# Optimization experiments

Measured on AMD Instinct MI355X. Metric: run time of the kernel, lower is better.

## Reference

```python
import jax, jax.numpy as jnp
import numpy as np
import math

FEAT_DIM = 128
N_BANK = 1000000
K_NEG = 4096
BATCH = 256
T = 0.5
MOMENTUM = 0.5
EPS = 1e-7


def setup_inputs() -> dict:
    key = jax.random.key(0)
    k1, k2, k3, k4, k5, k6 = jax.random.split(key, 6)
    stdv = 1.0 / math.sqrt(FEAT_DIM / 3)
    memory_l = jax.random.uniform(k1, (N_BANK, FEAT_DIM), minval=-stdv, maxval=stdv, dtype=jnp.float32)
    memory_ab = jax.random.uniform(k2, (N_BANK, FEAT_DIM), minval=-stdv, maxval=stdv, dtype=jnp.float32)
    l = jax.random.normal(k3, (BATCH, FEAT_DIM), dtype=jnp.float32)
    ab = jax.random.normal(k4, (BATCH, FEAT_DIM), dtype=jnp.float32)
    y = jax.random.randint(k5, (BATCH,), 0, N_BANK, dtype=jnp.int32)
    idx = jax.random.randint(k6, (BATCH, K_NEG + 1), 0, N_BANK, dtype=jnp.int32)
    idx = idx.at[:, 0].set(y)  # positive sample in slot 0, as in torch forward
    return {"l": l, "ab": ab, "memory_l": memory_l, "memory_ab": memory_ab, "y": y, "idx": idx}


def _l2_normalize(x):
    # matches torch: x / (sqrt(sum(x^2)) + eps)
    return x / (jnp.sqrt(jnp.sum(x * x, axis=1, keepdims=True)) + EPS)


def _momentum_update(memory, y, x_norm):
    # gather rows, momentum mix, renormalize, scatter back
    pos = memory[y] * MOMENTUM + x_norm * (1.0 - MOMENTUM)          # [B, D]
    norm = jnp.sqrt(jnp.sum(pos * pos, axis=1, keepdims=True))
    return memory.at[y].set(pos / norm)


def reference(l, ab, memory_l, memory_ab, y, idx):
    outputSize = memory_l.shape[0]
    ln = _l2_normalize(l)
    abn = _l2_normalize(ab)

    # gather negatives+positive from the AB bank, score against l features
    w_ab = jax.lax.stop_gradient(memory_ab[idx])                     # [B, K+1, D]
    P_l = jnp.exp(jnp.einsum('bkd,bd->bk', w_ab, ln) / T)[..., None]  # [B, K+1, 1]
    Z_l = jnp.mean(P_l) * outputSize
    out_l = P_l / Z_l

    w_l = jax.lax.stop_gradient(memory_l[idx])                       # [B, K+1, D]
    P_ab = jnp.exp(jnp.einsum('bkd,bd->bk', w_l, abn) / T)[..., None]
    Z_ab = jnp.mean(P_ab) * outputSize
    out_ab = P_ab / Z_ab

    # momentum scatter update of the memory banks (no_grad in torch)
    new_memory_l = jax.lax.stop_gradient(_momentum_update(memory_l, y, ln))
    new_memory_ab = jax.lax.stop_gradient(_momentum_update(memory_ab, y, abn))

    return out_l, out_ab, new_memory_l, new_memory_ab
```

## Files before the change

kernel.cpp:

```cpp
#include <hip/hip_runtime.h>
#include <math.h>
#include <stdint.h>

#define FEAT   128
#define NBANK  1000000
#define KP1    4097
#define BATCH  256
#define INV_T  2.0f
#define EPS_N  1e-7f

constexpr size_t TOTP   = (size_t)BATCH * KP1;
constexpr size_t O_OUTL = 0;
constexpr size_t O_OUTA = TOTP;
constexpr size_t O_MEML = 2 * TOTP;
constexpr size_t O_MEMA = O_MEML + (size_t)NBANK * FEAT;

constexpr int RPB   = 16;
constexpr int NBUCK = NBANK / RPB;
constexpr int CAP   = 128;

constexpr size_t WS_LN   = 0;
constexpr size_t WS_ABN  = 32768;
constexpr size_t WS_INVZ = 65536;
constexpr size_t WS_PL   = 65544;
constexpr size_t WS_PA   = 65800;
constexpr size_t WS_U32  = 66560;

typedef float vfloat4 __attribute__((ext_vector_type(4)));

__device__ __forceinline__ float dot4(vfloat4 a, vfloat4 b) {
    return a.x * b.x + a.y * b.y + a.z * b.z + a.w * b.w;
}

__global__ void norm_zero_kernel(const float* __restrict__ l,
                                 const float* __restrict__ ab,
                                 float* __restrict__ ws,
                                 unsigned int* __restrict__ cnt) {
    int b    = blockIdx.x;
    int lane = threadIdx.x;
    for (int i = b * 64 + lane; i < NBUCK; i += 512 * 64) cnt[i] = 0u;
    const float* src;
    float*       dst;
    if (b < BATCH) { src = l  + (size_t)b * FEAT;            dst = ws + WS_LN  + (size_t)b * FEAT; }
    else           { src = ab + (size_t)(b - BATCH) * FEAT;  dst = ws + WS_ABN + (size_t)(b - BATCH) * FEAT; }
    float2 v = *(const float2*)(src + 2 * lane);
    float  ss = v.x * v.x + v.y * v.y;
    #pragma unroll
    for (int m = 1; m < 64; m <<= 1) ss += __shfl_xor(ss, m, 64);
    float inv = 1.0f / (sqrtf(ss) + EPS_N);
    ((float2*)dst)[lane] = make_float2(v.x * inv, v.y * inv);
}

__global__ void build_kernel(const int* __restrict__ idx,
                             unsigned int* __restrict__ cnt,
                             unsigned int* __restrict__ ent) {
    size_t stride = (size_t)gridDim.x * blockDim.x;
    for (size_t p = (size_t)blockIdx.x * blockDim.x + threadIdx.x; p < TOTP; p += stride) {
        int row = idx[p];
        int b   = (int)(p / KP1);
        int k   = (int)(p - (size_t)b * KP1);
        int bucket = row >> 4;
        unsigned int pos = atomicAdd(&cnt[bucket], 1u);
        if (pos < (unsigned int)CAP)
            ent[(size_t)bucket * CAP + pos] =
                ((unsigned int)b << 17) | ((unsigned int)k << 4) | (unsigned int)(row & 15);
    }
}

__global__ __launch_bounds__(256) void main_kernel(
        const float* __restrict__ mem_l, const float* __restrict__ mem_ab,
        const float* __restrict__ ws_f,
        const unsigned int* __restrict__ cnt,
        const unsigned int* __restrict__ ent,
        float* __restrict__ out) {
    __shared__ float ldsL[RPB * FEAT];
    __shared__ float ldsA[RPB * FEAT];
    __shared__ unsigned int sEnt[CAP];
    int blk = blockIdx.x;
    int tid = threadIdx.x;
    size_t fbase = (size_t)blk * RPB * FEAT;

    int c = min((int)cnt[blk], CAP);
    if (tid < CAP && tid < c) sEnt[tid] = ent[(size_t)blk * CAP + tid];

    const vfloat4* sl = (const vfloat4*)(mem_l  + fbase);
    const vfloat4* sa = (const vfloat4*)(mem_ab + fbase);
    vfloat4 vl[2], va[2];
    #pragma unroll
    for (int j = 0; j < 2; ++j) vl[j] = sl[j * 256 + tid];
    #pragma unroll
    for (int j = 0; j < 2; ++j) va[j] = sa[j * 256 + tid];

    vfloat4* lL = (vfloat4*)ldsL;
    vfloat4* lA = (vfloat4*)ldsA;
    #pragma unroll
    for (int j = 0; j < 2; ++j) { int i = j * 256 + tid; lL[i] = vl[j]; lA[i] = va[j]; }
    __syncthreads();

    vfloat4* dl_ = (vfloat4*)(out + O_MEML + fbase);
    vfloat4* da_ = (vfloat4*)(out + O_MEMA + fbase);
    #pragma unroll
    for (int j = 0; j < 2; ++j) { int i = j * 256 + tid; dl_[i] = vl[j]; da_[i] = va[j]; }

    int g = tid >> 4, lane16 = tid & 15;
    for (int i = g; i < c; i += 16) {
        unsigned int ev = sEnt[i];
        int rloc = (int)(ev & 15u);
        int k    = (int)((ev >> 4) & 0x1FFFu);
        int b    = (int)(ev >> 17);
        const vfloat4* ra = (const vfloat4*)(ldsA + rloc * FEAT) + lane16 * 2;
        const vfloat4* rl = (const vfloat4*)(ldsL + rloc * FEAT) + lane16 * 2;
        vfloat4 wa0 = ra[0], wa1 = ra[1];
        vfloat4 wl0 = rl[0], wl1 = rl[1];
        const vfloat4* lq = (const vfloat4*)(ws_f + WS_LN  + (size_t)b * FEAT) + lane16 * 2;
        const vfloat4* aq = (const vfloat4*)(ws_f + WS_ABN + (size_t)b * FEAT) + lane16 * 2;
        vfloat4 lv0 = lq[0], lv1 = lq[1];
        vfloat4 av0 = aq[0], av1 = aq[1];
        float dl  = dot4(wa0, lv0) + dot4(wa1, lv1);
        float dab = dot4(wl0, av0) + dot4(wl1, av1);
        #pragma unroll
        for (int m = 1; m < 16; m <<= 1) {
            dl  += __shfl_xor(dl,  m, 64);
            dab += __shfl_xor(dab, m, 64);
        }
        if (lane16 == 0) {
            out[O_OUTL + (size_t)b * KP1 + k] = __expf(dl  * INV_T);
            out[O_OUTA + (size_t)b * KP1 + k] = __expf(dab * INV_T);
        }
    }
}

__global__ void zsum_kernel(const float* __restrict__ out,
                            float* __restrict__ pl, float* __restrict__ pa) {
    __shared__ float sl[256], sa[256];
    int i = blockIdx.x, t = threadIdx.x;
    const float* bl = out + O_OUTL + (size_t)i * KP1;
    const float* ba = out + O_OUTA + (size_t)i * KP1;
    float a = 0.f, b = 0.f;
    for (int p = t; p < KP1; p += 256) { a += bl[p]; b += ba[p]; }
    sl[t] = a; sa[t] = b;
    __syncthreads();
    for (int s = 128; s > 0; s >>= 1) {
        if (t < s) { sl[t] += sl[t + s]; sa[t] += sa[t + s]; }
        __syncthreads();
    }
    if (t == 0) { pl[i] = sl[0]; pa[i] = sa[0]; }
}

__global__ void zfinal_kernel(const float* __restrict__ pl,
                              const float* __restrict__ pa,
                              float* __restrict__ invz) {
    if (threadIdx.x == 0) {
        float a = 0.f, b = 0.f;
        for (int i = 0; i < 256; ++i) { a += pl[i]; b += pa[i]; }
        float count = (float)TOTP;
        invz[0] = count / (a * (float)NBANK);
        invz[1] = count / (b * (float)NBANK);
    }
}

__global__ void scale_kernel(float* __restrict__ out, const float* __restrict__ invz) {
    float zl = invz[0], za = invz[1];
    size_t stride = (size_t)gridDim.x * blockDim.x;
    for (size_t i = (size_t)blockIdx.x * blockDim.x + threadIdx.x; i < TOTP; i += stride) {
        out[O_OUTL + i] *= zl;
        out[O_OUTA + i] *= za;
    }
}

__global__ void update_kernel(const float* __restrict__ mem_l,
                              const float* __restrict__ mem_ab,
                              const int*   __restrict__ y,
                              const float* __restrict__ ws,
                              float* __restrict__ out) {
    int b    = blockIdx.x;
    int lane = threadIdx.x;
    int row  = y[b];
    for (int j = b + 1; j < BATCH; ++j)
        if (y[j] == row) return;
    {
        float2 m = ((const float2*)(mem_l + (size_t)row * FEAT))[lane];
        float2 x = ((const float2*)(ws + WS_LN + (size_t)b * FEAT))[lane];
        float2 p = make_float2(m.x * 0.5f + x.x * 0.5f, m.y * 0.5f + x.y * 0.5f);
        float ss = p.x * p.x + p.y * p.y;
        #pragma unroll
        for (int mk = 1; mk < 64; mk <<= 1) ss += __shfl_xor(ss, mk, 64);
        float nrm = sqrtf(ss);
        ((float2*)(out + O_MEML + (size_t)row * FEAT))[lane] =
            make_float2(p.x / nrm, p.y / nrm);
    }
    {
        float2 m = ((const float2*)(mem_ab + (size_t)row * FEAT))[lane];
        float2 x = ((const float2*)(ws + WS_ABN + (size_t)b * FEAT))[lane];
        float2 p = make_float2(m.x * 0.5f + x.x * 0.5f, m.y * 0.5f + x.y * 0.5f);
        float ss = p.x * p.x + p.y * p.y;
        #pragma unroll
        for (int mk = 1; mk < 64; mk <<= 1) ss += __shfl_xor(ss, mk, 64);
        float nrm = sqrtf(ss);
        ((float2*)(out + O_MEMA + (size_t)row * FEAT))[lane] =
            make_float2(p.x / nrm, p.y / nrm);
    }
}

extern "C" void kernel_launch(void* const* d_in, const int* in_sizes, int n_in,
                              void* d_out, int out_size, void* d_ws, size_t ws_size,
                              hipStream_t stream) {
    const float* l      = (const float*)d_in[0];
    const float* ab     = (const float*)d_in[1];
    const float* mem_l  = (const float*)d_in[2];
    const float* mem_ab = (const float*)d_in[3];
    const int*   y      = (const int*)d_in[4];
    const int*   idx    = (const int*)d_in[5];
    float* out = (float*)d_out;
    float* ws  = (float*)d_ws;

    unsigned int* wsu = (unsigned int*)(ws + WS_U32);
    unsigned int* cnt = wsu;
    unsigned int* ent = wsu + NBUCK;

    norm_zero_kernel<<<dim3(2 * BATCH), dim3(64), 0, stream>>>(l, ab, ws, cnt);
    build_kernel<<<dim3(2048), dim3(256), 0, stream>>>(idx, cnt, ent);
    main_kernel<<<dim3(NBUCK), dim3(256), 0, stream>>>(
        mem_l, mem_ab, ws, cnt, ent, out);
    zsum_kernel  <<<dim3(256), dim3(256), 0, stream>>>(out, ws + WS_PL, ws + WS_PA);
    zfinal_kernel<<<dim3(1),   dim3(64),  0, stream>>>(ws + WS_PL, ws + WS_PA, ws + WS_INVZ);
    scale_kernel<<<dim3(1024), dim3(256), 0, stream>>>(out, ws + WS_INVZ);
    update_kernel<<<dim3(BATCH), dim3(64), 0, stream>>>(mem_l, mem_ab, y, ws, out);
}
```

Measured before the change: 490.7 us.

## Bucket gather entries per row and use persistent grid-stride main kernel

```diff
diff --git a/kernel.cpp b/kernel.cpp
--- a/kernel.cpp
+++ b/kernel.cpp
@@ -15,9 +15,9 @@
 constexpr size_t O_MEML = 2 * TOTP;
 constexpr size_t O_MEMA = O_MEML + (size_t)NBANK * FEAT;
 
-constexpr int RPB   = 16;
-constexpr int NBUCK = NBANK / RPB;
-constexpr int CAP   = 128;
+constexpr int CAP    = 16;
+constexpr int NTILE  = NBANK / 16;
+constexpr int GRID_M = 2048;
 
 constexpr size_t WS_LN   = 0;
 constexpr size_t WS_ABN  = 32768;
@@ -38,7 +38,7 @@
                                  unsigned int* __restrict__ cnt) {
     int b    = blockIdx.x;
     int lane = threadIdx.x;
-    for (int i = b * 64 + lane; i < NBUCK; i += 512 * 64) cnt[i] = 0u;
+    for (int i = b * 64 + lane; i < NBANK; i += 512 * 64) cnt[i] = 0u;
     const float* src;
     float*       dst;
     if (b < BATCH) { src = l  + (size_t)b * FEAT;            dst = ws + WS_LN  + (size_t)b * FEAT; }
@@ -59,11 +59,9 @@
         int row = idx[p];
         int b   = (int)(p / KP1);
         int k   = (int)(p - (size_t)b * KP1);
-        int bucket = row >> 4;
-        unsigned int pos = atomicAdd(&cnt[bucket], 1u);
+        unsigned int pos = atomicAdd(&cnt[row], 1u);
         if (pos < (unsigned int)CAP)
-            ent[(size_t)bucket * CAP + pos] =
-                ((unsigned int)b << 17) | ((unsigned int)k << 4) | (unsigned int)(row & 15);
+            ent[(size_t)row * CAP + pos] = ((unsigned int)b << 13) | (unsigned int)k;
     }
 }
 
@@ -73,59 +71,45 @@
         const unsigned int* __restrict__ cnt,
         const unsigned int* __restrict__ ent,
         float* __restrict__ out) {
-    __shared__ float ldsL[RPB * FEAT];
-    __shared__ float ldsA[RPB * FEAT];
-    __shared__ unsigned int sEnt[CAP];
-    int blk = blockIdx.x;
-    int tid = threadIdx.x;
-    size_t fbase = (size_t)blk * RPB * FEAT;
-
-    int c = min((int)cnt[blk], CAP);
-    if (tid < CAP && tid < c) sEnt[tid] = ent[(size_t)blk * CAP + tid];
-
-    const vfloat4* sl = (const vfloat4*)(mem_l  + fbase);
-    const vfloat4* sa = (const vfloat4*)(mem_ab + fbase);
-    vfloat4 vl[2], va[2];
-    #pragma unroll
-    for (int j = 0; j < 2; ++j) vl[j] = sl[j * 256 + tid];
-    #pragma unroll
-    for (int j = 0; j < 2; ++j) va[j] = sa[j * 256 + tid];
-
-    vfloat4* lL = (vfloat4*)ldsL;
-    vfloat4* lA = (vfloat4*)ldsA;
-    #pragma unroll
-    for (int j = 0; j < 2; ++j) { int i = j * 256 + tid; lL[i] = vl[j]; lA[i] = va[j]; }
-    __syncthreads();
-
-    vfloat4* dl_ = (vfloat4*)(out + O_MEML + fbase);
-    vfloat4* da_ = (vfloat4*)(out + O_MEMA + fbase);
-    #pragma unroll
-    for (int j = 0; j < 2; ++j) { int i = j * 256 + tid; dl_[i] = vl[j]; da_[i] = va[j]; }
-
-    int g = tid >> 4, lane16 = tid & 15;
-    for (int i = g; i < c; i += 16) {
-        unsigned int ev = sEnt[i];
-        int rloc = (int)(ev & 15u);
-        int k    = (int)((ev >> 4) & 0x1FFFu);
-        int b    = (int)(ev >> 17);
-        const vfloat4* ra = (const vfloat4*)(ldsA + rloc * FEAT) + lane16 * 2;
-        const vfloat4* rl = (const vfloat4*)(ldsL + rloc * FEAT) + lane16 * 2;
-        vfloat4 wa0 = ra[0], wa1 = ra[1];
-        vfloat4 wl0 = rl[0], wl1 = rl[1];
-        const vfloat4* lq = (const vfloat4*)(ws_f + WS_LN  + (size_t)b * FEAT) + lane16 * 2;
-        const vfloat4* aq = (const vfloat4*)(ws_f + WS_ABN + (size_t)b * FEAT) + lane16 * 2;
-        vfloat4 lv0 = lq[0], lv1 = lq[1];
-        vfloat4 av0 = aq[0], av1 = aq[1];
-        float dl  = dot4(wa0, lv0) + dot4(wa1, lv1);
-        float dab = dot4(wl0, av0) + dot4(wl1, av1);
-        #pragma unroll
-        for (int m = 1; m < 16; m <<= 1) {
-            dl  += __shfl_xor(dl,  m, 64);
-            dab += __shfl_xor(dab, m, 64);
-        }
-        if (lane16 == 0) {
-            out[O_OUTL + (size_t)b * KP1 + k] = __expf(dl  * INV_T);
-            out[O_OUTA + (size_t)b * KP1 + k] = __expf(dab * INV_T);
+    int tid    = threadIdx.x;
+    int g      = tid >> 4;
+    int lane16 = tid & 15;
+
+    for (int t = blockIdx.x; t < NTILE; t += GRID_M) {
+        int    row   = t * 16 + g;
+        size_t rbase = (size_t)row * FEAT;
+
+        int c = (int)cnt[row];
+
+        const vfloat4* pl = (const vfloat4*)(mem_l  + rbase) + lane16 * 2;
+        const vfloat4* pa = (const vfloat4*)(mem_ab + rbase) + lane16 * 2;
+        vfloat4 wl0 = pl[0], wl1 = pl[1];
+        vfloat4 wa0 = pa[0], wa1 = pa[1];
+
+        vfloat4* dl = (vfloat4*)(out + O_MEML + rbase) + lane16 * 2;
+        vfloat4* da = (vfloat4*)(out + O_MEMA + rbase) + lane16 * 2;
+        dl[0] = wl0; dl[1] = wl1;
+        da[0] = wa0; da[1] = wa1;
+
+        for (int e = 0; e < c && e < CAP; ++e) {
+            unsigned int ev = ent[(size_t)row * CAP + e];
+            int b = (int)(ev >> 13);
+            int k = (int)(ev & 0x1FFFu);
+            const vfloat4* lq = (const vfloat4*)(ws_f + WS_LN  + (size_t)b * FEAT) + lane16 * 2;
+            const vfloat4* aq = (const vfloat4*)(ws_f + WS_ABN + (size_t)b * FEAT) + lane16 * 2;
+            vfloat4 lv0 = lq[0], lv1 = lq[1];
+            vfloat4 av0 = aq[0], av1 = aq[1];
+            float dlv  = dot4(wa0, lv0) + dot4(wa1, lv1);
+            float dabv = dot4(wl0, av0) + dot4(wl1, av1);
+            #pragma unroll
+            for (int m = 1; m < 16; m <<= 1) {
+                dlv  += __shfl_xor(dlv,  m, 64);
+                dabv += __shfl_xor(dabv, m, 64);
+            }
+            if (lane16 == 0) {
+                out[O_OUTL + (size_t)b * KP1 + k] = __expf(dlv  * INV_T);
+                out[O_OUTA + (size_t)b * KP1 + k] = __expf(dabv * INV_T);
+            }
         }
     }
 }
@@ -216,11 +200,11 @@
 
     unsigned int* wsu = (unsigned int*)(ws + WS_U32);
     unsigned int* cnt = wsu;
-    unsigned int* ent = wsu + NBUCK;
+    unsigned int* ent = wsu + NBANK;
 
     norm_zero_kernel<<<dim3(2 * BATCH), dim3(64), 0, stream>>>(l, ab, ws, cnt);
     build_kernel<<<dim3(2048), dim3(256), 0, stream>>>(idx, cnt, ent);
-    main_kernel<<<dim3(NBUCK), dim3(256), 0, stream>>>(
+    main_kernel<<<dim3(GRID_M), dim3(256), 0, stream>>>(
         mem_l, mem_ab, ws, cnt, ent, out);
     zsum_kernel  <<<dim3(256), dim3(256), 0, stream>>>(out, ws + WS_PL, ws + WS_PA);
     zfinal_kernel<<<dim3(1),   dim3(64),  0, stream>>>(ws + WS_PL, ws + WS_PA, ws + WS_INVZ);
```

Result: slower. 679.0 us (+38.4%).

## Split bank copy+score per bank, drop LDS staging, fuse normalize with scatter update

Applied to the files above, without the earlier changes.

```diff
diff --git a/kernel.cpp b/kernel.cpp
--- a/kernel.cpp
+++ b/kernel.cpp
@@ -21,7 +21,6 @@
 
 constexpr size_t WS_LN   = 0;
 constexpr size_t WS_ABN  = 32768;
-constexpr size_t WS_INVZ = 65536;
 constexpr size_t WS_PL   = 65544;
 constexpr size_t WS_PA   = 65800;
 constexpr size_t WS_U32  = 66560;
@@ -67,66 +66,36 @@
     }
 }
 
-__global__ __launch_bounds__(256) void main_kernel(
-        const float* __restrict__ mem_l, const float* __restrict__ mem_ab,
-        const float* __restrict__ ws_f,
+__global__ __launch_bounds__(256) void copyscore_kernel(
+        const float* __restrict__ src, float* __restrict__ dst,
+        const float* __restrict__ qtab, float* __restrict__ pout,
         const unsigned int* __restrict__ cnt,
-        const unsigned int* __restrict__ ent,
-        float* __restrict__ out) {
-    __shared__ float ldsL[RPB * FEAT];
-    __shared__ float ldsA[RPB * FEAT];
-    __shared__ unsigned int sEnt[CAP];
+        const unsigned int* __restrict__ ent) {
     int blk = blockIdx.x;
     int tid = threadIdx.x;
     size_t fbase = (size_t)blk * RPB * FEAT;
 
     int c = min((int)cnt[blk], CAP);
-    if (tid < CAP && tid < c) sEnt[tid] = ent[(size_t)blk * CAP + tid];
 
-    const vfloat4* sl = (const vfloat4*)(mem_l  + fbase);
-    const vfloat4* sa = (const vfloat4*)(mem_ab + fbase);
-    vfloat4 vl[2], va[2];
-    #pragma unroll
-    for (int j = 0; j < 2; ++j) vl[j] = sl[j * 256 + tid];
-    #pragma unroll
-    for (int j = 0; j < 2; ++j) va[j] = sa[j * 256 + tid];
-
-    vfloat4* lL = (vfloat4*)ldsL;
-    vfloat4* lA = (vfloat4*)ldsA;
-    #pragma unroll
-    for (int j = 0; j < 2; ++j) { int i = j * 256 + tid; lL[i] = vl[j]; lA[i] = va[j]; }
-    __syncthreads();
-
-    vfloat4* dl_ = (vfloat4*)(out + O_MEML + fbase);
-    vfloat4* da_ = (vfloat4*)(out + O_MEMA + fbase);
-    #pragma unroll
-    for (int j = 0; j < 2; ++j) { int i = j * 256 + tid; dl_[i] = vl[j]; da_[i] = va[j]; }
+    const vfloat4* s = (const vfloat4*)(src + fbase);
+    vfloat4 v0 = s[tid], v1 = s[256 + tid];
+    vfloat4* d = (vfloat4*)(dst + fbase);
+    d[tid] = v0; d[256 + tid] = v1;
 
     int g = tid >> 4, lane16 = tid & 15;
     for (int i = g; i < c; i += 16) {
-        unsigned int ev = sEnt[i];
+        unsigned int ev = ent[(size_t)blk * CAP + i];
         int rloc = (int)(ev & 15u);
         int k    = (int)((ev >> 4) & 0x1FFFu);
         int b    = (int)(ev >> 17);
-        const vfloat4* ra = (const vfloat4*)(ldsA + rloc * FEAT) + lane16 * 2;
-        const vfloat4* rl = (const vfloat4*)(ldsL + rloc * FEAT) + lane16 * 2;
-        vfloat4 wa0 = ra[0], wa1 = ra[1];
-        vfloat4 wl0 = rl[0], wl1 = rl[1];
-        const vfloat4* lq = (const vfloat4*)(ws_f + WS_LN  + (size_t)b * FEAT) + lane16 * 2;
-        const vfloat4* aq = (const vfloat4*)(ws_f + WS_ABN + (size_t)b * FEAT) + lane16 * 2;
-        vfloat4 lv0 = lq[0], lv1 = lq[1];
-        vfloat4 av0 = aq[0], av1 = aq[1];
-        float dl  = dot4(wa0, lv0) + dot4(wa1, lv1);
-        float dab = dot4(wl0, av0) + dot4(wl1, av1);
+        const vfloat4* rp = (const vfloat4*)(src + fbase + (size_t)rloc * FEAT) + lane16 * 2;
+        vfloat4 w0 = rp[0], w1 = rp[1];
+        const vfloat4* qp = (const vfloat4*)(qtab + (size_t)b * FEAT) + lane16 * 2;
+        vfloat4 q0 = qp[0], q1 = qp[1];
+        float dv = dot4(w0, q0) + dot4(w1, q1);
         #pragma unroll
-        for (int m = 1; m < 16; m <<= 1) {
-            dl  += __shfl_xor(dl,  m, 64);
-            dab += __shfl_xor(dab, m, 64);
-        }
-        if (lane16 == 0) {
-            out[O_OUTL + (size_t)b * KP1 + k] = __expf(dl  * INV_T);
-            out[O_OUTA + (size_t)b * KP1 + k] = __expf(dab * INV_T);
-        }
+        for (int m = 1; m < 16; m <<= 1) dv += __shfl_xor(dv, m, 64);
+        if (lane16 == 0) pout[(size_t)b * KP1 + k] = __expf(dv * INV_T);
     }
 }
 
@@ -147,58 +116,58 @@
     if (t == 0) { pl[i] = sl[0]; pa[i] = sa[0]; }
 }
 
-__global__ void zfinal_kernel(const float* __restrict__ pl,
+__global__ void finish_kernel(const float* __restrict__ pl,
                               const float* __restrict__ pa,
-                              float* __restrict__ invz) {
-    if (threadIdx.x == 0) {
-        float a = 0.f, b = 0.f;
-        for (int i = 0; i < 256; ++i) { a += pl[i]; b += pa[i]; }
-        float count = (float)TOTP;
-        invz[0] = count / (a * (float)NBANK);
-        invz[1] = count / (b * (float)NBANK);
-    }
-}
-
-__global__ void scale_kernel(float* __restrict__ out, const float* __restrict__ invz) {
-    float zl = invz[0], za = invz[1];
-    size_t stride = (size_t)gridDim.x * blockDim.x;
-    for (size_t i = (size_t)blockIdx.x * blockDim.x + threadIdx.x; i < TOTP; i += stride) {
-        out[O_OUTL + i] *= zl;
-        out[O_OUTA + i] *= za;
-    }
-}
-
-__global__ void update_kernel(const float* __restrict__ mem_l,
+                              const float* __restrict__ mem_l,
                               const float* __restrict__ mem_ab,
                               const int*   __restrict__ y,
                               const float* __restrict__ ws,
                               float* __restrict__ out) {
-    int b    = blockIdx.x;
-    int lane = threadIdx.x;
-    int row  = y[b];
-    for (int j = b + 1; j < BATCH; ++j)
-        if (y[j] == row) return;
-    {
-        float2 m = ((const float2*)(mem_l + (size_t)row * FEAT))[lane];
-        float2 x = ((const float2*)(ws + WS_LN + (size_t)b * FEAT))[lane];
-        float2 p = make_float2(m.x * 0.5f + x.x * 0.5f, m.y * 0.5f + x.y * 0.5f);
-        float ss = p.x * p.x + p.y * p.y;
-        #pragma unroll
-        for (int mk = 1; mk < 64; mk <<= 1) ss += __shfl_xor(ss, mk, 64);
-        float nrm = sqrtf(ss);
-        ((float2*)(out + O_MEML + (size_t)row * FEAT))[lane] =
-            make_float2(p.x / nrm, p.y / nrm);
+    __shared__ float s2[2];
+    int b = blockIdx.x, t = threadIdx.x;
+    if (t == 0) {
+        float a = 0.f, c = 0.f;
+        for (int i = 0; i < 256; ++i) { a += pl[i]; c += pa[i]; }
+        float count = (float)TOTP;
+        s2[0] = count / (a * (float)NBANK);
+        s2[1] = count / (c * (float)NBANK);
     }
-    {
-        float2 m = ((const float2*)(mem_ab + (size_t)row * FEAT))[lane];
-        float2 x = ((const float2*)(ws + WS_ABN + (size_t)b * FEAT))[lane];
-        float2 p = make_float2(m.x * 0.5f + x.x * 0.5f, m.y * 0.5f + x.y * 0.5f);
-        float ss = p.x * p.x + p.y * p.y;
-        #pragma unroll
-        for (int mk = 1; mk < 64; mk <<= 1) ss += __shfl_xor(ss, mk, 64);
-        float nrm = sqrtf(ss);
-        ((float2*)(out + O_MEMA + (size_t)row * FEAT))[lane] =
-            make_float2(p.x / nrm, p.y / nrm);
+    __syncthreads();
+    float zl = s2[0], za = s2[1];
+    float* bl = out + O_OUTL + (size_t)b * KP1;
+    float* ba = out + O_OUTA + (size_t)b * KP1;
+    for (int p = t; p < KP1; p += 256) { bl[p] *= zl; ba[p] *= za; }
+
+    if (t < 64) {
+        int lane = t;
+        int row  = y[b];
+        bool win = true;
+        for (int j = b + 1; j < BATCH; ++j)
+            if (y[j] == row) { win = false; break; }
+        if (win) {
+            {
+                float2 m = ((const float2*)(mem_l + (size_t)row * FEAT))[lane];
+                float2 x = ((const float2*)(ws + WS_LN + (size_t)b * FEAT))[lane];
+                float2 p = make_float2(m.x * 0.5f + x.x * 0.5f, m.y * 0.5f + x.y * 0.5f);
+                float ss = p.x * p.x + p.y * p.y;
+                #pragma unroll
+                for (int mk = 1; mk < 64; mk <<= 1) ss += __shfl_xor(ss, mk, 64);
+                float nrm = sqrtf(ss);
+                ((float2*)(out + O_MEML + (size_t)row * FEAT))[lane] =
+                    make_float2(p.x / nrm, p.y / nrm);
+            }
+            {
+                float2 m = ((const float2*)(mem_ab + (size_t)row * FEAT))[lane];
+                float2 x = ((const float2*)(ws + WS_ABN + (size_t)b * FEAT))[lane];
+                float2 p = make_float2(m.x * 0.5f + x.x * 0.5f, m.y * 0.5f + x.y * 0.5f);
+                float ss = p.x * p.x + p.y * p.y;
+                #pragma unroll
+                for (int mk = 1; mk < 64; mk <<= 1) ss += __shfl_xor(ss, mk, 64);
+                float nrm = sqrtf(ss);
+                ((float2*)(out + O_MEMA + (size_t)row * FEAT))[lane] =
+                    make_float2(p.x / nrm, p.y / nrm);
+            }
+        }
     }
 }
 
@@ -220,10 +189,11 @@
 
     norm_zero_kernel<<<dim3(2 * BATCH), dim3(64), 0, stream>>>(l, ab, ws, cnt);
     build_kernel<<<dim3(2048), dim3(256), 0, stream>>>(idx, cnt, ent);
-    main_kernel<<<dim3(NBUCK), dim3(256), 0, stream>>>(
-        mem_l, mem_ab, ws, cnt, ent, out);
-    zsum_kernel  <<<dim3(256), dim3(256), 0, stream>>>(out, ws + WS_PL, ws + WS_PA);
-    zfinal_kernel<<<dim3(1),   dim3(64),  0, stream>>>(ws + WS_PL, ws + WS_PA, ws + WS_INVZ);
-    scale_kernel<<<dim3(1024), dim3(256), 0, stream>>>(out, ws + WS_INVZ);
-    update_kernel<<<dim3(BATCH), dim3(64), 0, stream>>>(mem_l, mem_ab, y, ws, out);
+    copyscore_kernel<<<dim3(NBUCK), dim3(256), 0, stream>>>(
+        mem_l, out + O_MEML, ws + WS_ABN, out + O_OUTA, cnt, ent);
+    copyscore_kernel<<<dim3(NBUCK), dim3(256), 0, stream>>>(
+        mem_ab, out + O_MEMA, ws + WS_LN, out + O_OUTL, cnt, ent);
+    zsum_kernel<<<dim3(256), dim3(256), 0, stream>>>(out, ws + WS_PL, ws + WS_PA);
+    finish_kernel<<<dim3(BATCH), dim3(256), 0, stream>>>(
+        ws + WS_PL, ws + WS_PA, mem_l, mem_ab, y, ws, out);
 }
```

Measured after the change: 515.7 us. +5.1%, slower.
